# Performance work log

Hardware: AMD Instinct MI355X
Metric: run time of the kernel (lower is better)

The kernel has to match this reference:

```python
import jax, jax.numpy as jnp
import numpy as np

S, B, H, NH = 2048, 4, 1024, 16
HD = H // NH
MASK_VAL = -10000.0

def setup_inputs() -> dict:
    key = jax.random.key(0)
    ks = jax.random.split(key, 6)
    hidden_states = jax.random.normal(ks[0], (S, B, H), dtype=jnp.float32)
    attention_mask = jax.random.randint(ks[1], (B, 1, S, S), 0, 2).astype(bool)
    W_qkv = jax.random.normal(ks[2], (3 * H, H), dtype=jnp.float32) * (H ** -0.5)
    b_qkv = jax.random.normal(ks[3], (3 * H,), dtype=jnp.float32) * 0.02
    W_dense = jax.random.normal(ks[4], (H, H), dtype=jnp.float32) * (H ** -0.5)
    b_dense = jax.random.normal(ks[5], (H,), dtype=jnp.float32) * 0.02
    return {"hidden_states": hidden_states, "attention_mask": attention_mask,
            "W_qkv": W_qkv, "b_qkv": b_qkv, "W_dense": W_dense, "b_dense": b_dense}

def reference(hidden_states, attention_mask, W_qkv, b_qkv, W_dense, b_dense):
    # QKV projection: [s,b,h] -> [s,b,3h] -> [s,b,NH,3*HD], split last dim into q,k,v
    mixed = hidden_states @ W_qkv.T + b_qkv
    mixed = mixed.reshape(S, B, NH, 3 * HD)
    q, k, v = mixed[..., :HD], mixed[..., HD:2 * HD], mixed[..., 2 * HD:]
    norm_factor = jnp.float32(1.0 / np.sqrt(HD))
    # scores: [b, nh, sq, sk] (baddbmm beta=0.7 on torch.empty is undefined; baseline treated as 0)
    scores = jnp.einsum('sbhd,tbhd->bhst', q, k) * norm_factor
    scores = jnp.where(attention_mask, MASK_VAL, scores)
    probs = jax.nn.softmax(scores, axis=-1)
    # attention dropout (p=0.7) omitted for deterministic reference (eval mode)
    ctx = jnp.einsum('bhst,tbhd->sbhd', probs, v)  # [s,b,nh,hd]
    ctx = ctx.reshape(S, B, H)
    out = ctx @ W_dense.T + b_dense
    return out
```

## Files before the change

kernel.cpp:

```cpp
#include <hip/hip_runtime.h>
#include <hip/hip_bf16.h>
#include <math.h>

constexpr int S_ = 2048, B_ = 4, H_ = 1024, NH_ = 16, HD_ = 64;

typedef __attribute__((ext_vector_type(8))) short short8;
typedef __attribute__((ext_vector_type(4))) short short4v;
typedef __attribute__((ext_vector_type(4))) float floatx4;
typedef __attribute__((ext_vector_type(2))) unsigned uint2v;

static __device__ __forceinline__ short f2bf(float f) {
    union { float f; unsigned u; } v; v.f = f;
    unsigned r = v.u + 0x7FFFu + ((v.u >> 16) & 1u);
    return (short)(r >> 16);
}

static __device__ __forceinline__ unsigned pack_bf(float p0, float p1) {
    return __builtin_amdgcn_perm(__float_as_uint(p1), __float_as_uint(p0), 0x07060302u);
}

static __device__ __forceinline__ void gl2lds16(const void* g, void* l) {
    __builtin_amdgcn_global_load_lds(
        (const __attribute__((address_space(1))) void*)g,
        (__attribute__((address_space(3))) void*)l, 16, 0, 0);
}

static __device__ __forceinline__ short8 pswz(unsigned a0, unsigned a1,
                                              unsigned b0, unsigned b1) {
    uint2v r0 = __builtin_amdgcn_permlane32_swap(a0, b0, false, false);
    uint2v s0 = __builtin_amdgcn_permlane16_swap(r0.x, r0.y, false, false);
    uint2v r1 = __builtin_amdgcn_permlane32_swap(a1, b1, false, false);
    uint2v s1 = __builtin_amdgcn_permlane16_swap(r1.x, r1.y, false, false);
    union { unsigned u[4]; short8 s; } o;
    o.u[0] = s0.x;
    o.u[1] = s1.x;
    o.u[2] = s0.y;
    o.u[3] = s1.y;
    return o.s;
}

__global__ __launch_bounds__(256) void cvt3_kernel(
    const float* __restrict__ a, short* __restrict__ oa, int na,
    const float* __restrict__ b, short* __restrict__ ob, int nb,
    const float* __restrict__ c, short* __restrict__ oc, int nc)
{
    const int idx = blockIdx.x * 256 + threadIdx.x;
    const float* src; short* dst; int i;
    if (idx < na)            { src = a; dst = oa; i = idx; }
    else if (idx < na + nb)  { src = b; dst = ob; i = idx - na; }
    else                     { src = c; dst = oc; i = idx - na - nb; }
    const float4 v = ((const float4*)src)[i];
    short4v o = { (short)f2bf(v.x), (short)f2bf(v.y), (short)f2bf(v.z), (short)f2bf(v.w) };
    ((short4v*)dst)[i] = o;
}

__global__ __launch_bounds__(256) void mask_u8_kernel(
    const int* __restrict__ m, unsigned* __restrict__ mb)
{
    const int i = blockIdx.x * 256 + threadIdx.x;
    const int4 v = ((const int4*)m)[i];
    unsigned r = (v.x ? 0u : 0xFFu)      | (v.y ? 0u : 0xFF00u) |
                 (v.z ? 0u : 0xFF0000u)  | (v.w ? 0u : 0xFF000000u);
    mb[i] = r;
}

__global__ __launch_bounds__(256, 3) void gemm_qkv_mfma(
    const short* __restrict__ A, const short* __restrict__ Bw,
    const float* __restrict__ bias,
    short* __restrict__ Qb, short* __restrict__ Kb, short* __restrict__ Vb)
{
    constexpr int K = H_;
    __shared__ __align__(16) short As[3 * 4096];
    __shared__ __align__(16) short Bs[3 * 4096];

    const int t = threadIdx.x;
    const int wave = t >> 6, lane = t & 63;
    const int l15 = lane & 15, quad = lane >> 4;
    const int wm = wave & 1, wn = wave >> 1;
    const int row0 = blockIdx.y * 128;
    const int col0 = blockIdx.x * 128;

    floatx4 acc[4][4];
#pragma unroll
    for (int mi = 0; mi < 4; ++mi)
#pragma unroll
        for (int ni = 0; ni < 4; ++ni)
            acc[mi][ni] = (floatx4){0.f, 0.f, 0.f, 0.f};

    const int c0 = wave * 128 + lane, c1 = c0 + 64;
    const int r0 = c0 >> 2, jg0 = (((c0 & 3) ^ (((r0 & 3) + ((r0 >> 2) & 3)) & 3))) * 8;
    const int r1 = c1 >> 2, jg1 = (((c1 & 3) ^ (((r1 & 3) + ((r1 >> 2) & 3)) & 3))) * 8;
    const int db0 = (wave * 128) * 8;
    const int db1 = db0 + 64 * 8;

    const short* Ar0 = A  + (size_t)(row0 + r0) * K + jg0;
    const short* Ar1 = A  + (size_t)(row0 + r1) * K + jg1;
    const short* Br0 = Bw + (size_t)(col0 + r0) * K + jg0;
    const short* Br1 = Bw + (size_t)(col0 + r1) * K + jg1;

    gl2lds16(Ar0, &As[db0]); gl2lds16(Ar1, &As[db1]);
    gl2lds16(Br0, &Bs[db0]); gl2lds16(Br1, &Bs[db1]);
    __builtin_amdgcn_sched_barrier(0);
    gl2lds16(Ar0 + 32, &As[4096 + db0]); gl2lds16(Ar1 + 32, &As[4096 + db1]);
    gl2lds16(Br0 + 32, &Bs[4096 + db0]); gl2lds16(Br1 + 32, &Bs[4096 + db1]);
    __builtin_amdgcn_sched_barrier(0);

    int bc = 0, bs = 2;
#pragma unroll 1
    for (int it = 0; it < 32; ++it) {
        if (it < 31) { asm volatile("s_waitcnt vmcnt(4)" ::: "memory"); }
        else         { asm volatile("s_waitcnt vmcnt(0)" ::: "memory"); }
        __builtin_amdgcn_s_barrier();
        __builtin_amdgcn_sched_barrier(0);

        if (it < 30) {
            const int ko = (it + 2) * 32;
            gl2lds16(Ar0 + ko, &As[bs * 4096 + db0]);
            gl2lds16(Ar1 + ko, &As[bs * 4096 + db1]);
            gl2lds16(Br0 + ko, &Bs[bs * 4096 + db0]);
            gl2lds16(Br1 + ko, &Bs[bs * 4096 + db1]);
        }
        __builtin_amdgcn_sched_barrier(0);

        const int bo = bc * 4096;
        short8 af[4], bfr[4];
#pragma unroll
        for (int mi = 0; mi < 4; ++mi) {
            const int R = wm * 64 + mi * 16 + l15;
            const int sel = quad ^ (((R & 3) + ((R >> 2) & 3)) & 3);
            af[mi] = *(const short8*)&As[bo + R * 32 + sel * 8];
        }
#pragma unroll
        for (int ni = 0; ni < 4; ++ni) {
            const int R = wn * 64 + ni * 16 + l15;
            const int sel = quad ^ (((R & 3) + ((R >> 2) & 3)) & 3);
            bfr[ni] = *(const short8*)&Bs[bo + R * 32 + sel * 8];
        }
        __builtin_amdgcn_s_setprio(1);
#pragma unroll
        for (int mi = 0; mi < 4; ++mi)
#pragma unroll
            for (int ni = 0; ni < 4; ++ni)
                acc[mi][ni] = __builtin_amdgcn_mfma_f32_16x16x32_bf16(
                    af[mi], bfr[ni], acc[mi][ni], 0, 0, 0);
        __builtin_amdgcn_s_setprio(0);

        bc = (bc == 2) ? 0 : bc + 1;
        bs = (bs == 2) ? 0 : bs + 1;
    }

#pragma unroll
    for (int ni = 0; ni < 4; ++ni) {
        const int gc = col0 + wn * 64 + ni * 16 + l15;
        const float bv = bias[gc];
        const int hh = gc / 192;
        const int rem = gc - hh * 192;
        const int which = rem >> 6, d = rem & 63;
#pragma unroll
        for (int mi = 0; mi < 4; ++mi)
#pragma unroll
            for (int i = 0; i < 4; ++i) {
                const int gr = row0 + wm * 64 + mi * 16 + quad * 4 + i;
                const int s = gr >> 2, bb = gr & 3;
                float fv = acc[mi][ni][i] + bv;
                const size_t ho = (size_t)(bb * NH_ + hh);
                if (which == 0)      Qb[(ho * S_ + s) * HD_ + d] = f2bf(fv * 0.1803368801111204f);
                else if (which == 1) Kb[(ho * S_ + s) * HD_ + d] = f2bf(fv);
                else                 Vb[(ho * S_ + s) * HD_ + d] = f2bf(fv);
            }
    }
}

__global__ __launch_bounds__(256) void vtrans_kernel(
    const short* __restrict__ Vb, short* __restrict__ Vtb)
{
    const int bh = blockIdx.y;
    const int s0 = blockIdx.x * 64;
    __shared__ __align__(16) short T[64 * 64];
    const int t = threadIdx.x;

#pragma unroll
    for (int it = 0; it < 2; ++it) {
        const int c = t + it * 256;
        const int r = c >> 3, jp = c & 7;
        const int jg = jp ^ ((r >> 3) & 7);
        *(short8*)&T[r * 64 + jp * 8] =
            *(const short8*)(Vb + ((size_t)bh * S_ + s0 + r) * HD_ + jg * 8);
    }
    __syncthreads();

#pragma unroll
    for (int it = 0; it < 2; ++it) {
        const int c = t + it * 256;
        const int d = c >> 3, sg = (c & 7) * 8;
        short8 v;
#pragma unroll
        for (int k = 0; k < 8; ++k) {
            const int r = sg + k;
            v[k] = T[r * 64 + (((d >> 3) ^ ((r >> 3) & 7)) * 8) + (d & 7)];
        }
        *(short8*)(Vtb + ((size_t)bh * HD_ + d) * S_ + s0 + sg) = v;
    }
}

__global__ __launch_bounds__(256, 3) void gemm_dense_mfma(
    const short* __restrict__ A, const short* __restrict__ Bw,
    const float* __restrict__ bias, float* __restrict__ out)
{
    constexpr int K = H_;
    __shared__ __align__(16) short As[3 * 4096];
    __shared__ __align__(16) short Bs[3 * 4096];

    const int t = threadIdx.x;
    const int wave = t >> 6, lane = t & 63;
    const int l15 = lane & 15, quad = lane >> 4;
    const int wm = wave & 1, wn = wave >> 1;
    const int row0 = blockIdx.y * 128;
    const int col0 = blockIdx.x * 128;

    floatx4 acc[4][4];
#pragma unroll
    for (int mi = 0; mi < 4; ++mi)
#pragma unroll
        for (int ni = 0; ni < 4; ++ni)
            acc[mi][ni] = (floatx4){0.f, 0.f, 0.f, 0.f};

    const int c0 = wave * 128 + lane, c1 = c0 + 64;
    const int r0 = c0 >> 2, jg0 = (((c0 & 3) ^ (((r0 & 3) + ((r0 >> 2) & 3)) & 3))) * 8;
    const int r1 = c1 >> 2, jg1 = (((c1 & 3) ^ (((r1 & 3) + ((r1 >> 2) & 3)) & 3))) * 8;
    const int db0 = (wave * 128) * 8;
    const int db1 = db0 + 64 * 8;

    const short* Ar0 = A  + (size_t)(row0 + r0) * K + jg0;
    const short* Ar1 = A  + (size_t)(row0 + r1) * K + jg1;
    const short* Br0 = Bw + (size_t)(col0 + r0) * K + jg0;
    const short* Br1 = Bw + (size_t)(col0 + r1) * K + jg1;

    gl2lds16(Ar0, &As[db0]); gl2lds16(Ar1, &As[db1]);
    gl2lds16(Br0, &Bs[db0]); gl2lds16(Br1, &Bs[db1]);
    __builtin_amdgcn_sched_barrier(0);
    gl2lds16(Ar0 + 32, &As[4096 + db0]); gl2lds16(Ar1 + 32, &As[4096 + db1]);
    gl2lds16(Br0 + 32, &Bs[4096 + db0]); gl2lds16(Br1 + 32, &Bs[4096 + db1]);
    __builtin_amdgcn_sched_barrier(0);

    int bc = 0, bs = 2;
#pragma unroll 1
    for (int it = 0; it < 32; ++it) {
        if (it < 31) { asm volatile("s_waitcnt vmcnt(4)" ::: "memory"); }
        else         { asm volatile("s_waitcnt vmcnt(0)" ::: "memory"); }
        __builtin_amdgcn_s_barrier();
        __builtin_amdgcn_sched_barrier(0);

        if (it < 30) {
            const int ko = (it + 2) * 32;
            gl2lds16(Ar0 + ko, &As[bs * 4096 + db0]);
            gl2lds16(Ar1 + ko, &As[bs * 4096 + db1]);
            gl2lds16(Br0 + ko, &Bs[bs * 4096 + db0]);
            gl2lds16(Br1 + ko, &Bs[bs * 4096 + db1]);
        }
        __builtin_amdgcn_sched_barrier(0);

        const int bo = bc * 4096;
        short8 af[4], bfr[4];
#pragma unroll
        for (int mi = 0; mi < 4; ++mi) {
            const int R = wm * 64 + mi * 16 + l15;
            const int sel = quad ^ (((R & 3) + ((R >> 2) & 3)) & 3);
            af[mi] = *(const short8*)&As[bo + R * 32 + sel * 8];
        }
#pragma unroll
        for (int ni = 0; ni < 4; ++ni) {
            const int R = wn * 64 + ni * 16 + l15;
            const int sel = quad ^ (((R & 3) + ((R >> 2) & 3)) & 3);
            bfr[ni] = *(const short8*)&Bs[bo + R * 32 + sel * 8];
        }
        __builtin_amdgcn_s_setprio(1);
#pragma unroll
        for (int mi = 0; mi < 4; ++mi)
#pragma unroll
            for (int ni = 0; ni < 4; ++ni)
                acc[mi][ni] = __builtin_amdgcn_mfma_f32_16x16x32_bf16(
                    af[mi], bfr[ni], acc[mi][ni], 0, 0, 0);
        __builtin_amdgcn_s_setprio(0);

        bc = (bc == 2) ? 0 : bc + 1;
        bs = (bs == 2) ? 0 : bs + 1;
    }

#pragma unroll
    for (int ni = 0; ni < 4; ++ni) {
        const int gc = col0 + wn * 64 + ni * 16 + l15;
        const float bv = bias[gc];
#pragma unroll
        for (int mi = 0; mi < 4; ++mi)
#pragma unroll
            for (int i = 0; i < 4; ++i) {
                const int gr = row0 + wm * 64 + mi * 16 + quad * 4 + i;
                out[(size_t)gr * H_ + gc] = acc[mi][ni][i] + bv;
            }
    }
}

__global__ __launch_bounds__(256, 2) void flash_mfma_kernel(
    const short* __restrict__ Qb, const short* __restrict__ Kb,
    const short* __restrict__ Vtb, const unsigned char* __restrict__ mask8,
    short* __restrict__ ctxb)
{
    const int bh = blockIdx.y;
    const int b  = bh >> 4;
    const int h  = bh & 15;
    const int s0 = blockIdx.x * 128;

    const int tdx  = threadIdx.x;
    const int wave = tdx >> 6;
    const int lane = tdx & 63;
    const int l15  = lane & 15;
    const int quad = lane >> 4;

    __shared__ __align__(16) short Ks [3 * 4096];
    __shared__ __align__(16) short Vts[3 * 4096];
    __shared__ __align__(16) unsigned char Ms[3 * 8192];

    const short* Qg = Qb + ((size_t)bh * S_ + s0 + wave * 32 + l15) * HD_;
    short8 qf00 = *(const short8*)(Qg + quad * 8);
    short8 qf01 = *(const short8*)(Qg + 32 + quad * 8);
    short8 qf10 = *(const short8*)(Qg + 16 * HD_ + quad * 8);
    short8 qf11 = *(const short8*)(Qg + 16 * HD_ + 32 + quad * 8);

    const short* Kbase  = Kb  + (size_t)bh * S_ * HD_;
    const short* Vtbase = Vtb + (size_t)bh * HD_ * S_;

    floatx4 o[2][4];
    floatx4 lacc[2];
#pragma unroll
    for (int g = 0; g < 2; ++g) {
        lacc[g] = (floatx4){0.f, 0.f, 0.f, 0.f};
#pragma unroll
        for (int n0 = 0; n0 < 4; ++n0) o[g][n0] = (floatx4){0.f, 0.f, 0.f, 0.f};
    }
    const short8 ones8 = {(short)0x3F80, (short)0x3F80, (short)0x3F80, (short)0x3F80,
                          (short)0x3F80, (short)0x3F80, (short)0x3F80, (short)0x3F80};

    const int cb0 = wave * 64, cb1 = (4 + wave) * 64;
    const int c0 = cb0 + lane,  c1 = cb1 + lane;
    const int r0 = c0 >> 3, jg0 = ((c0 & 7) ^ (r0 & 7)) * 8;
    const int r1 = c1 >> 3, jg1 = ((c1 & 7) ^ (r1 & 7)) * 8;

    const int mq0 = wave * 32 + (lane >> 2);
    const int mq1 = mq0 + 16;
    const int msw0 = (mq0 & 3) ^ ((mq0 >> 2) & 3);
    const int msw1 = (mq1 & 3) ^ ((mq1 >> 2) & 3);
    const unsigned char* msrc0 = mask8 + ((size_t)b * S_ + s0 + mq0) * S_ + ((lane & 3) ^ msw0) * 16;
    const unsigned char* msrc1 = mask8 + ((size_t)b * S_ + s0 + mq1) * S_ + ((lane & 3) ^ msw1) * 16;
    const int mdst0 = wave * 2048;
    const int mdst1 = wave * 2048 + 1024;

    const int sq = (l15 & 3) ^ (l15 >> 2);
    const int mrd0 = (wave * 32 + l15) * 64 + quad * 4;
    const int mrd1 = (wave * 32 + 16 + l15) * 64 + quad * 4;

    gl2lds16(Kbase  + (size_t)r0 * HD_ + jg0, &Ks[cb0 * 8]);
    gl2lds16(Kbase  + (size_t)r1 * HD_ + jg1, &Ks[cb1 * 8]);
    gl2lds16(Vtbase + (size_t)r0 * S_ + jg0,  &Vts[cb0 * 8]);
    gl2lds16(Vtbase + (size_t)r1 * S_ + jg1,  &Vts[cb1 * 8]);
    gl2lds16(msrc0, &Ms[mdst0]);
    gl2lds16(msrc1, &Ms[mdst1]);
    __builtin_amdgcn_sched_barrier(0);
    gl2lds16(Kbase  + (size_t)(64 + r0) * HD_ + jg0, &Ks[4096 + cb0 * 8]);
    gl2lds16(Kbase  + (size_t)(64 + r1) * HD_ + jg1, &Ks[4096 + cb1 * 8]);
    gl2lds16(Vtbase + (size_t)r0 * S_ + 64 + jg0,    &Vts[4096 + cb0 * 8]);
    gl2lds16(Vtbase + (size_t)r1 * S_ + 64 + jg1,    &Vts[4096 + cb1 * 8]);
    gl2lds16(msrc0 + 64, &Ms[8192 + mdst0]);
    gl2lds16(msrc1 + 64, &Ms[8192 + mdst1]);
    __builtin_amdgcn_sched_barrier(0);

    const floatx4 z4 = {0.f, 0.f, 0.f, 0.f};
    int bc = 0, bs = 2;

#pragma unroll 1
    for (int it = 0; it < 32; ++it) {
        if (it < 31) { asm volatile("s_waitcnt vmcnt(6)" ::: "memory"); }
        else         { asm volatile("s_waitcnt vmcnt(0)" ::: "memory"); }
        __builtin_amdgcn_s_barrier();
        __builtin_amdgcn_sched_barrier(0);

        if (it < 30) {
            const size_t tn = (size_t)(it + 2) * 64;
            gl2lds16(Kbase  + (tn + r0) * HD_ + jg0,      &Ks[bs * 4096 + cb0 * 8]);
            gl2lds16(Kbase  + (tn + r1) * HD_ + jg1,      &Ks[bs * 4096 + cb1 * 8]);
            gl2lds16(Vtbase + (size_t)r0 * S_ + tn + jg0, &Vts[bs * 4096 + cb0 * 8]);
            gl2lds16(Vtbase + (size_t)r1 * S_ + tn + jg1, &Vts[bs * 4096 + cb1 * 8]);
            gl2lds16(msrc0 + tn, &Ms[bs * 8192 + mdst0]);
            gl2lds16(msrc1 + tn, &Ms[bs * 8192 + mdst1]);
        }
        __builtin_amdgcn_sched_barrier(0);

        const int bo = bc * 4096;
        const int mo = bc * 8192;
        floatx4 sc[2][4];
        __builtin_amdgcn_s_setprio(1);
#pragma unroll
        for (int n0 = 0; n0 < 4; ++n0) {
            const int R = n0 * 16 + l15, xr = R & 7;
            const short8 kb0 = *(const short8*)&Ks[bo + R * 64 + ((quad ^ xr) * 8)];
            const short8 kb1 = *(const short8*)&Ks[bo + R * 64 + (((quad + 4) ^ xr) * 8)];
            sc[0][n0] = __builtin_amdgcn_mfma_f32_16x16x32_bf16(kb0, qf00, z4, 0, 0, 0);
            sc[0][n0] = __builtin_amdgcn_mfma_f32_16x16x32_bf16(kb1, qf01, sc[0][n0], 0, 0, 0);
            sc[1][n0] = __builtin_amdgcn_mfma_f32_16x16x32_bf16(kb0, qf10, z4, 0, 0, 0);
            sc[1][n0] = __builtin_amdgcn_mfma_f32_16x16x32_bf16(kb1, qf11, sc[1][n0], 0, 0, 0);
        }
        __builtin_amdgcn_s_setprio(0);

        unsigned uu[2][4][2];
#pragma unroll
        for (int g = 0; g < 2; ++g) {
            const int mrd = g ? mrd1 : mrd0;
#pragma unroll
            for (int n0 = 0; n0 < 4; ++n0) {
                const unsigned mw = *(const unsigned*)&Ms[mo + mrd + ((n0 ^ sq) << 4)];
                const floatx4 v = sc[g][n0];
                const unsigned q0 = __builtin_amdgcn_perm(0u, mw, 0x01010000u);
                const unsigned q1 = __builtin_amdgcn_perm(0u, mw, 0x03030202u);
                const unsigned u0 = pack_bf(__builtin_amdgcn_exp2f(v[0]),
                                            __builtin_amdgcn_exp2f(v[1])) & q0;
                const unsigned u1 = pack_bf(__builtin_amdgcn_exp2f(v[2]),
                                            __builtin_amdgcn_exp2f(v[3])) & q1;
                uu[g][n0][0] = u0; uu[g][n0][1] = u1;
            }
        }
        short8 pa00 = pswz(uu[0][0][0], uu[0][0][1], uu[0][1][0], uu[0][1][1]);
        short8 pa01 = pswz(uu[0][2][0], uu[0][2][1], uu[0][3][0], uu[0][3][1]);
        short8 pa10 = pswz(uu[1][0][0], uu[1][0][1], uu[1][1][0], uu[1][1][1]);
        short8 pa11 = pswz(uu[1][2][0], uu[1][2][1], uu[1][3][0], uu[1][3][1]);

        __builtin_amdgcn_s_setprio(1);
        lacc[0] = __builtin_amdgcn_mfma_f32_16x16x32_bf16(pa00, ones8, lacc[0], 0, 0, 0);
        lacc[0] = __builtin_amdgcn_mfma_f32_16x16x32_bf16(pa01, ones8, lacc[0], 0, 0, 0);
        lacc[1] = __builtin_amdgcn_mfma_f32_16x16x32_bf16(pa10, ones8, lacc[1], 0, 0, 0);
        lacc[1] = __builtin_amdgcn_mfma_f32_16x16x32_bf16(pa11, ones8, lacc[1], 0, 0, 0);
#pragma unroll
        for (int n0 = 0; n0 < 4; ++n0) {
            const int R = n0 * 16 + l15, xr = R & 7;
            const short8 vb0 = *(const short8*)&Vts[bo + R * 64 + ((quad ^ xr) * 8)];
            const short8 vb1 = *(const short8*)&Vts[bo + R * 64 + (((quad + 4) ^ xr) * 8)];
            o[0][n0] = __builtin_amdgcn_mfma_f32_16x16x32_bf16(pa00, vb0, o[0][n0], 0, 0, 0);
            o[0][n0] = __builtin_amdgcn_mfma_f32_16x16x32_bf16(pa01, vb1, o[0][n0], 0, 0, 0);
            o[1][n0] = __builtin_amdgcn_mfma_f32_16x16x32_bf16(pa10, vb0, o[1][n0], 0, 0, 0);
            o[1][n0] = __builtin_amdgcn_mfma_f32_16x16x32_bf16(pa11, vb1, o[1][n0], 0, 0, 0);
        }
        __builtin_amdgcn_s_setprio(0);

        bc = (bc == 2) ? 0 : bc + 1;
        bs = (bs == 2) ? 0 : bs + 1;
    }

#pragma unroll
    for (int g = 0; g < 2; ++g) {
#pragma unroll
        for (int i = 0; i < 4; ++i) {
            const float la = 1.f / lacc[g][i];
            const int sA = s0 + wave * 32 + g * 16 + quad * 4 + i;
#pragma unroll
            for (int n0 = 0; n0 < 4; ++n0)
                ctxb[((size_t)sA * B_ + b) * H_ + h * HD_ + n0 * 16 + l15] =
                    f2bf(o[g][n0][i] * la);
        }
    }
}

extern "C" void kernel_launch(void* const* d_in, const int* in_sizes, int n_in,
                              void* d_out, int out_size, void* d_ws, size_t ws_size,
                              hipStream_t stream)
{
    const float* hidden = (const float*)d_in[0];
    const int*   mask   = (const int*)d_in[1];
    const float* Wqkv   = (const float*)d_in[2];
    const float* bqkv   = (const float*)d_in[3];
    const float* Wd     = (const float*)d_in[4];
    const float* bd     = (const float*)d_in[5];
    float* out = (float*)d_out;

    const size_t HE = (size_t)B_ * NH_ * S_ * HD_;
    short* hBF    = (short*)d_ws;
    short* WqkvBF = hBF + (size_t)S_ * B_ * H_;
    short* WdBF   = WqkvBF + (size_t)3 * H_ * H_;
    short* Qb     = WdBF + (size_t)H_ * H_;
    short* Kb     = Qb + HE;
    short* Vb     = Kb + HE;
    short* Vtb    = Vb + HE;
    short* ctxb   = Vtb + HE;
    unsigned char* mask8 = (unsigned char*)hBF;

    const int nh4 = (S_ * B_ * H_) / 4;
    const int nw4 = (3 * H_ * H_) / 4;
    const int nd4 = (H_ * H_) / 4;
    hipLaunchKernelGGL(cvt3_kernel, dim3((nh4 + nw4 + nd4) / 256), dim3(256), 0, stream,
                       hidden, hBF, nh4, Wqkv, WqkvBF, nw4, Wd, WdBF, nd4);

    hipLaunchKernelGGL(gemm_qkv_mfma, dim3((3 * H_) / 128, (S_ * B_) / 128), dim3(256), 0, stream,
                       hBF, WqkvBF, bqkv, Qb, Kb, Vb);
    hipLaunchKernelGGL(mask_u8_kernel, dim3((B_ * S_ * S_ / 4) / 256), dim3(256), 0, stream,
                       mask, (unsigned*)mask8);
    hipLaunchKernelGGL(vtrans_kernel, dim3(S_ / 64, B_ * NH_), dim3(256), 0, stream,
                       Vb, Vtb);
    hipLaunchKernelGGL(flash_mfma_kernel, dim3(S_ / 128, B_ * NH_), dim3(256), 0, stream,
                       Qb, Kb, Vtb, mask8, ctxb);
    hipLaunchKernelGGL(gemm_dense_mfma, dim3(H_ / 128, (S_ * B_) / 128), dim3(256), 0, stream,
                       ctxb, WdBF, bd, out);
}
```

Before: 360.1 us.

## Pack attention mask into bitmasks and double flash block to 8 waves

Replaces the byte-per-element mask with a 64-bit ballot bitmask laid out per key tile, so the flash kernel loads one eighth of the mask bytes. A small LDS lookup table expands each 4-bit nibble into bf16 lane masks. The flash kernel now runs 512 threads covering 256 query rows, so each K/V tile staged in LDS is shared by twice as many waves and each thread issues fewer loads. Risks include the lookup-table and shift overhead in the softmax inner loop, lower occupancy from the larger block (the launch bound now asks for 4 blocks of 512 threads per CU), and the mask-packing kernel's ballot pattern reading global memory less efficiently.

Result: no change. 361.0 us (+0.3%).

```diff
diff --git a/kernel.cpp b/kernel.cpp
--- a/kernel.cpp
+++ b/kernel.cpp
@@ -23,6 +23,11 @@
     __builtin_amdgcn_global_load_lds(
         (const __attribute__((address_space(1))) void*)g,
         (__attribute__((address_space(3))) void*)l, 16, 0, 0);
+}
+static __device__ __forceinline__ void gl2lds4(const void* g, void* l) {
+    __builtin_amdgcn_global_load_lds(
+        (const __attribute__((address_space(1))) void*)g,
+        (__attribute__((address_space(3))) void*)l, 4, 0, 0);
 }
 
 static __device__ __forceinline__ short8 pswz(unsigned a0, unsigned a1,
@@ -54,14 +59,18 @@
     ((short4v*)dst)[i] = o;
 }
 
-__global__ __launch_bounds__(256) void mask_u8_kernel(
-    const int* __restrict__ m, unsigned* __restrict__ mb)
-{
-    const int i = blockIdx.x * 256 + threadIdx.x;
-    const int4 v = ((const int4*)m)[i];
-    unsigned r = (v.x ? 0u : 0xFFu)      | (v.y ? 0u : 0xFF00u) |
-                 (v.z ? 0u : 0xFF0000u)  | (v.w ? 0u : 0xFF000000u);
-    mb[i] = r;
+__global__ __launch_bounds__(256) void mask_bit_kernel(
+    const int* __restrict__ m, unsigned long long* __restrict__ mb)
+{
+    const int wid  = blockIdx.x * 4 + (threadIdx.x >> 6);
+    const int lane = threadIdx.x & 63;
+    const int b   = wid >> 16;
+    const int rem = wid & 65535;
+    const int q   = rem >> 5;
+    const int tb  = rem & 31;
+    const int v = m[((size_t)b * S_ + q) * S_ + tb * 64 + lane];
+    const unsigned long long w = __ballot(v == 0);
+    if (lane == 0) mb[((size_t)b * 32 + tb) * 2048 + q] = w;
 }
 
 __global__ __launch_bounds__(256, 3) void gemm_qkv_mfma(
@@ -301,15 +310,15 @@
     }
 }
 
-__global__ __launch_bounds__(256, 2) void flash_mfma_kernel(
+__global__ __launch_bounds__(512, 4) void flash_mfma_kernel(
     const short* __restrict__ Qb, const short* __restrict__ Kb,
-    const short* __restrict__ Vtb, const unsigned char* __restrict__ mask8,
+    const short* __restrict__ Vtb, const unsigned long long* __restrict__ mbits,
     short* __restrict__ ctxb)
 {
     const int bh = blockIdx.y;
     const int b  = bh >> 4;
     const int h  = bh & 15;
-    const int s0 = blockIdx.x * 128;
+    const int s0 = blockIdx.x * 256;
 
     const int tdx  = threadIdx.x;
     const int wave = tdx >> 6;
@@ -319,7 +328,15 @@
 
     __shared__ __align__(16) short Ks [3 * 4096];
     __shared__ __align__(16) short Vts[3 * 4096];
-    __shared__ __align__(16) unsigned char Ms[3 * 8192];
+    __shared__ __align__(16) uint2v Mb[3 * 256];
+    __shared__ __align__(16) uint2v Mlut[16];
+
+    if (tdx < 16) {
+        const unsigned m0 = ((tdx & 1) ? 0xFFFFu : 0u) | ((tdx & 2) ? 0xFFFF0000u : 0u);
+        const unsigned m1 = ((tdx & 4) ? 0xFFFFu : 0u) | ((tdx & 8) ? 0xFFFF0000u : 0u);
+        Mlut[tdx] = (uint2v){m0, m1};
+    }
+    __syncthreads();
 
     const short* Qg = Qb + ((size_t)bh * S_ + s0 + wave * 32 + l15) * HD_;
     short8 qf00 = *(const short8*)(Qg + quad * 8);
@@ -341,62 +358,41 @@
     const short8 ones8 = {(short)0x3F80, (short)0x3F80, (short)0x3F80, (short)0x3F80,
                           (short)0x3F80, (short)0x3F80, (short)0x3F80, (short)0x3F80};
 
-    const int cb0 = wave * 64, cb1 = (4 + wave) * 64;
-    const int c0 = cb0 + lane,  c1 = cb1 + lane;
+    const int c0 = wave * 64 + lane;
     const int r0 = c0 >> 3, jg0 = ((c0 & 7) ^ (r0 & 7)) * 8;
-    const int r1 = c1 >> 3, jg1 = ((c1 & 7) ^ (r1 & 7)) * 8;
-
-    const int mq0 = wave * 32 + (lane >> 2);
-    const int mq1 = mq0 + 16;
-    const int msw0 = (mq0 & 3) ^ ((mq0 >> 2) & 3);
-    const int msw1 = (mq1 & 3) ^ ((mq1 >> 2) & 3);
-    const unsigned char* msrc0 = mask8 + ((size_t)b * S_ + s0 + mq0) * S_ + ((lane & 3) ^ msw0) * 16;
-    const unsigned char* msrc1 = mask8 + ((size_t)b * S_ + s0 + mq1) * S_ + ((lane & 3) ^ msw1) * 16;
-    const int mdst0 = wave * 2048;
-    const int mdst1 = wave * 2048 + 1024;
-
-    const int sq = (l15 & 3) ^ (l15 >> 2);
-    const int mrd0 = (wave * 32 + l15) * 64 + quad * 4;
-    const int mrd1 = (wave * 32 + 16 + l15) * 64 + quad * 4;
-
-    gl2lds16(Kbase  + (size_t)r0 * HD_ + jg0, &Ks[cb0 * 8]);
-    gl2lds16(Kbase  + (size_t)r1 * HD_ + jg1, &Ks[cb1 * 8]);
-    gl2lds16(Vtbase + (size_t)r0 * S_ + jg0,  &Vts[cb0 * 8]);
-    gl2lds16(Vtbase + (size_t)r1 * S_ + jg1,  &Vts[cb1 * 8]);
-    gl2lds16(msrc0, &Ms[mdst0]);
-    gl2lds16(msrc1, &Ms[mdst1]);
+    const int kvdst = wave * 512;
+    const char* msrc = (const char*)mbits + ((size_t)(b * 32) * 2048 + s0 + wave * 32) * 8 + lane * 4;
+    const int   mdst = wave * 256;
+
+    gl2lds16(Kbase  + (size_t)r0 * HD_ + jg0, &Ks[kvdst]);
+    gl2lds16(Vtbase + (size_t)r0 * S_ + jg0,  &Vts[kvdst]);
+    gl2lds4 (msrc,                            (char*)Mb + mdst);
     __builtin_amdgcn_sched_barrier(0);
-    gl2lds16(Kbase  + (size_t)(64 + r0) * HD_ + jg0, &Ks[4096 + cb0 * 8]);
-    gl2lds16(Kbase  + (size_t)(64 + r1) * HD_ + jg1, &Ks[4096 + cb1 * 8]);
-    gl2lds16(Vtbase + (size_t)r0 * S_ + 64 + jg0,    &Vts[4096 + cb0 * 8]);
-    gl2lds16(Vtbase + (size_t)r1 * S_ + 64 + jg1,    &Vts[4096 + cb1 * 8]);
-    gl2lds16(msrc0 + 64, &Ms[8192 + mdst0]);
-    gl2lds16(msrc1 + 64, &Ms[8192 + mdst1]);
+    gl2lds16(Kbase  + (size_t)(64 + r0) * HD_ + jg0, &Ks[4096 + kvdst]);
+    gl2lds16(Vtbase + (size_t)r0 * S_ + 64 + jg0,    &Vts[4096 + kvdst]);
+    gl2lds4 (msrc + 2048 * 8,                        (char*)Mb + 2048 + mdst);
     __builtin_amdgcn_sched_barrier(0);
 
     const floatx4 z4 = {0.f, 0.f, 0.f, 0.f};
+    const int qsh = quad * 4;
     int bc = 0, bs = 2;
 
 #pragma unroll 1
     for (int it = 0; it < 32; ++it) {
-        if (it < 31) { asm volatile("s_waitcnt vmcnt(6)" ::: "memory"); }
+        if (it < 31) { asm volatile("s_waitcnt vmcnt(3)" ::: "memory"); }
         else         { asm volatile("s_waitcnt vmcnt(0)" ::: "memory"); }
         __builtin_amdgcn_s_barrier();
         __builtin_amdgcn_sched_barrier(0);
 
         if (it < 30) {
             const size_t tn = (size_t)(it + 2) * 64;
-            gl2lds16(Kbase  + (tn + r0) * HD_ + jg0,      &Ks[bs * 4096 + cb0 * 8]);
-            gl2lds16(Kbase  + (tn + r1) * HD_ + jg1,      &Ks[bs * 4096 + cb1 * 8]);
-            gl2lds16(Vtbase + (size_t)r0 * S_ + tn + jg0, &Vts[bs * 4096 + cb0 * 8]);
-            gl2lds16(Vtbase + (size_t)r1 * S_ + tn + jg1, &Vts[bs * 4096 + cb1 * 8]);
-            gl2lds16(msrc0 + tn, &Ms[bs * 8192 + mdst0]);
-            gl2lds16(msrc1 + tn, &Ms[bs * 8192 + mdst1]);
+            gl2lds16(Kbase  + (tn + r0) * HD_ + jg0,      &Ks[bs * 4096 + kvdst]);
+            gl2lds16(Vtbase + (size_t)r0 * S_ + tn + jg0, &Vts[bs * 4096 + kvdst]);
+            gl2lds4 (msrc + (size_t)(it + 2) * 2048 * 8,  (char*)Mb + bs * 2048 + mdst);
         }
         __builtin_amdgcn_sched_barrier(0);
 
         const int bo = bc * 4096;
-        const int mo = bc * 8192;
         floatx4 sc[2][4];
         __builtin_amdgcn_s_setprio(1);
 #pragma unroll
@@ -411,20 +407,23 @@
         }
         __builtin_amdgcn_s_setprio(0);
 
+        const uint2v row0b = Mb[bc * 256 + wave * 32 + l15];
+        const uint2v row1b = Mb[bc * 256 + wave * 32 + 16 + l15];
+
         unsigned uu[2][4][2];
 #pragma unroll
         for (int g = 0; g < 2; ++g) {
-            const int mrd = g ? mrd1 : mrd0;
+            const uint2v rw = g ? row1b : row0b;
 #pragma unroll
             for (int n0 = 0; n0 < 4; ++n0) {
-                const unsigned mw = *(const unsigned*)&Ms[mo + mrd + ((n0 ^ sq) << 4)];
+                const unsigned selw = (n0 < 2) ? rw.x : rw.y;
+                const unsigned nib = (selw >> (qsh + ((n0 & 1) << 4))) & 15u;
+                const uint2v mm = Mlut[nib];
                 const floatx4 v = sc[g][n0];
-                const unsigned q0 = __builtin_amdgcn_perm(0u, mw, 0x01010000u);
-                const unsigned q1 = __builtin_amdgcn_perm(0u, mw, 0x03030202u);
                 const unsigned u0 = pack_bf(__builtin_amdgcn_exp2f(v[0]),
-                                            __builtin_amdgcn_exp2f(v[1])) & q0;
+                                            __builtin_amdgcn_exp2f(v[1])) & mm.x;
                 const unsigned u1 = pack_bf(__builtin_amdgcn_exp2f(v[2]),
-                                            __builtin_amdgcn_exp2f(v[3])) & q1;
+                                            __builtin_amdgcn_exp2f(v[3])) & mm.y;
                 uu[g][n0][0] = u0; uu[g][n0][1] = u1;
             }
         }
@@ -489,7 +488,7 @@
     short* Vb     = Kb + HE;
     short* Vtb    = Vb + HE;
     short* ctxb   = Vtb + HE;
-    unsigned char* mask8 = (unsigned char*)hBF;
+    unsigned long long* mbits = (unsigned long long*)hBF;
 
     const int nh4 = (S_ * B_ * H_) / 4;
     const int nw4 = (3 * H_ * H_) / 4;
@@ -499,12 +498,12 @@
 
     hipLaunchKernelGGL(gemm_qkv_mfma, dim3((3 * H_) / 128, (S_ * B_) / 128), dim3(256), 0, stream,
                        hBF, WqkvBF, bqkv, Qb, Kb, Vb);
-    hipLaunchKernelGGL(mask_u8_kernel, dim3((B_ * S_ * S_ / 4) / 256), dim3(256), 0, stream,
-                       mask, (unsigned*)mask8);
+    hipLaunchKernelGGL(mask_bit_kernel, dim3(B_ * S_ * 32 / 4), dim3(256), 0, stream,
+                       mask, mbits);
     hipLaunchKernelGGL(vtrans_kernel, dim3(S_ / 64, B_ * NH_), dim3(256), 0, stream,
                        Vb, Vtb);
-    hipLaunchKernelGGL(flash_mfma_kernel, dim3(S_ / 128, B_ * NH_), dim3(256), 0, stream,
-                       Qb, Kb, Vtb, mask8, ctxb);
+    hipLaunchKernelGGL(flash_mfma_kernel, dim3(S_ / 256, B_ * NH_), dim3(512), 0, stream,
+                       Qb, Kb, Vtb, mbits, ctxb);
     hipLaunchKernelGGL(gemm_dense_mfma, dim3(H_ / 128, (S_ * B_) / 128), dim3(256), 0, stream,
                        ctxb, WdBF, bd, out);
 }
```
